# Kernel optimization log

Measured on AMD Instinct MI355X. Metric: run time of the kernel, lower is better.

The kernel has to match this reference:

```python
import jax, jax.numpy as jnp
import numpy as np

KH = KW = 3
STRIDE = 1
PAD = 1
DIL = 1


def _conv2d(x, w, b):
    out = jax.lax.conv_general_dilated(
        x, w, (STRIDE, STRIDE), [(PAD, PAD), (PAD, PAD)],
        rhs_dilation=(DIL, DIL), dimension_numbers=('NCHW', 'OIHW', 'NCHW'))
    return out + b[None, :, None, None]


def _bilinear_sample(x, ys, xs):
    # x: [B,C,H,W]; ys, xs: [B,K,Ho,Wo] float sampling coords (zero padding outside)
    B, C, H, W = x.shape
    y0 = jnp.floor(ys)
    x0 = jnp.floor(xs)
    wy1 = ys - y0
    wx1 = xs - x0
    wy0 = 1.0 - wy1
    wx0 = 1.0 - wx1
    x_flat = x.reshape(B, C, H * W)

    def gather(yc, xc):
        valid = (yc >= 0) & (yc <= H - 1) & (xc >= 0) & (xc <= W - 1)
        yi = jnp.clip(yc, 0, H - 1).astype(jnp.int32)
        xi = jnp.clip(xc, 0, W - 1).astype(jnp.int32)
        idx = yi * W + xi  # [B,K,Ho,Wo]
        g = jax.vmap(lambda xb, ib: xb[:, ib.reshape(-1)])(x_flat, idx)
        g = g.reshape(B, C, *idx.shape[1:])  # [B,C,K,Ho,Wo]
        return g * valid[:, None].astype(x.dtype)

    return (gather(y0, x0) * (wy0 * wx0)[:, None]
            + gather(y0, x0 + 1) * (wy0 * wx1)[:, None]
            + gather(y0 + 1, x0) * (wy1 * wx0)[:, None]
            + gather(y0 + 1, x0 + 1) * (wy1 * wx1)[:, None])


def setup_inputs() -> dict:
    key = jax.random.key(0)
    ks = jax.random.split(key, 6)
    B, C, H, W = 8, 256, 64, 64
    Cout = 256
    K = KH * KW
    x = jax.random.normal(ks[0], (B, C, H, W), jnp.float32)
    # small random offset/mask heads (module inits them to zero; random keeps the
    # irregular-gather path exercised with modest, realistic offsets)
    w_offset = jax.random.normal(ks[1], (2 * K, C, KH, KW), jnp.float32) * 0.01
    b_offset = jax.random.normal(ks[2], (2 * K,), jnp.float32) * 0.1
    w_mask = jax.random.normal(ks[3], (K, C, KH, KW), jnp.float32) * 0.01
    b_mask = jnp.zeros((K,), jnp.float32)
    stdv = 1.0 / np.sqrt(C * KH * KW)
    weight = jax.random.uniform(ks[4], (Cout, C, KH, KW), jnp.float32, -stdv, stdv)
    bias = jnp.zeros((Cout,), jnp.float32)
    return {"x": x, "w_offset": w_offset, "b_offset": b_offset,
            "w_mask": w_mask, "b_mask": b_mask, "weight": weight, "bias": bias}


def reference(x, w_offset, b_offset, w_mask, b_mask, weight, bias):
    B, C, H, W = x.shape
    K = KH * KW
    offset = _conv2d(x, w_offset, b_offset)          # [B, 2K, Ho, Wo]
    mask = jax.nn.sigmoid(_conv2d(x, w_mask, b_mask))  # [B, K, Ho, Wo]
    Ho, Wo = offset.shape[2], offset.shape[3]
    off = offset.reshape(B, K, 2, Ho, Wo)
    dy, dx = off[:, :, 0], off[:, :, 1]              # (dy, dx) pairs per kernel tap
    ky = jnp.arange(KH, dtype=x.dtype) * DIL - PAD
    kx = jnp.arange(KW, dtype=x.dtype) * DIL - PAD
    kyf = jnp.repeat(ky, KW)   # [K]
    kxf = jnp.tile(kx, KH)     # [K]
    ys = jnp.arange(Ho, dtype=x.dtype)[None, None, :, None] * STRIDE + kyf[None, :, None, None] + dy
    xs = jnp.arange(Wo, dtype=x.dtype)[None, None, None, :] * STRIDE + kxf[None, :, None, None] + dx
    sampled = _bilinear_sample(x, ys, xs) * mask[:, None]  # [B,C,K,Ho,Wo]
    out = jnp.einsum('bckhw,ock->bohw', sampled, weight.reshape(weight.shape[0], C, K))
    return out + bias[None, :, None, None]
```

## Files before the change

### kernel.cpp

```cpp
#include <hip/hip_runtime.h>
#include <math.h>


typedef __bf16 bf16x8 __attribute__((ext_vector_type(8)));
typedef float  f32x4  __attribute__((ext_vector_type(4)));
typedef float  f32x2  __attribute__((ext_vector_type(2)));
typedef int    i32x4  __attribute__((ext_vector_type(4)));
typedef unsigned short u16x8 __attribute__((ext_vector_type(8)));
typedef unsigned short u16x4 __attribute__((ext_vector_type(4)));

__device__ __forceinline__ unsigned short f2b(float f) {
  return __builtin_bit_cast(unsigned short, (__bf16)f);
}
__device__ __forceinline__ float blo(unsigned u) {
  return __builtin_bit_cast(float, u << 16);
}
__device__ __forceinline__ float bhi(unsigned u) {
  return __builtin_bit_cast(float, u & 0xffff0000u);
}

__global__ __launch_bounds__(256) void prep(const float* __restrict__ x,
                                            unsigned short* __restrict__ xt,
                                            const float* __restrict__ w,
                                            const float* __restrict__ wo,
                                            const float* __restrict__ wm,
                                            __bf16* __restrict__ wp,
                                            __bf16* __restrict__ womp) {
  __shared__ float tile[64][65];
  const int t = threadIdx.x;
  if (blockIdx.x < 2048) {
    const int bid = blockIdx.x;
    const int b = bid & 7, rem = bid >> 3;
    const int cc = rem & 3, hw0 = (rem >> 2) << 6;
    const int a = t & 63, g = t >> 6;
#pragma unroll
    for (int r = 0; r < 16; ++r) {
      int crow = (r << 2) + g;
      tile[crow][a] = x[(((b << 8) + (cc << 6) + crow) << 12) + hw0 + a];
    }
    __syncthreads();
    const int a0 = (t & 15) << 2, gg = t >> 4;
#pragma unroll
    for (int r = 0; r < 4; ++r) {
      int hwr = (r << 4) + gg;
      u16x4 v;
#pragma unroll
      for (int j = 0; j < 4; ++j) v[j] = f2b(tile[a0 + j][hwr]);
      *(u16x4*)&xt[((b << 12) + hw0 + hwr) * 256 + (cc << 6) + a0] = v;
    }
  } else if (blockIdx.x < 4352) {
    int idx = (blockIdx.x - 2048) * 256 + t;
    int o = idx / 2304, rem = idx - o * 2304;
    int c = rem / 9, k = rem - c * 9;
    wp[(((k << 5) + (c >> 3)) * 256 + o) * 8 + (c & 7)] = (__bf16)w[idx];
  } else {
    int idx = (blockIdx.x - 4352) * 256 + t;
    if (idx >= 32 * 256 * 9) return;
    int r = idx / 2304, rem = idx - r * 2304;
    int c = rem / 9, k = rem - c * 9;
    float v = 0.f;
    if (r < 18) v = wo[((r << 8) + c) * 9 + k];
    else if (r < 27) v = wm[(((r - 18) << 8) + c) * 9 + k];
    womp[(((k << 5) + (c >> 3)) * 32 + r) * 8 + (c & 7)] = (__bf16)v;
  }
}

__global__ __launch_bounds__(512, 2) void deform_fused(
    const unsigned short* __restrict__ xt, const __bf16* __restrict__ wp,
    const __bf16* __restrict__ womp, const float* __restrict__ b_off,
    const float* __restrict__ b_msk, const float* __restrict__ bias,
    float* __restrict__ out) {
  const int bi = blockIdx.x & 7, h = blockIdx.x >> 3;
  const int t = threadIdx.x, lane = t & 63, wv = t >> 6;
  const int l16 = lane & 15, lh = lane >> 4;
  __shared__ __align__(16) unsigned short S[2][64 * 64];
  __shared__ __align__(16) float samp[9][64][8];
  __shared__ __align__(16) float offm[27][64];

  const int sp = t >> 3;
  const int sc0 = (t & 7) << 3;
  const int wofs = (sp << 6) + ((((t & 7) ^ (sp & 7)) & 7) << 3);
  const unsigned short* xtb = xt + ((long)bi << 20);

  {
    f32x4 oacc = {};
    const int mf = wv & 1, nf = wv >> 1;

    auto POLOAD = [&](int it, u16x8* r) {
      const int k = it >> 2, cc = it & 3;
      const int hh = h + k / 3 - 1;
      const int ww = sp + (k % 3) - 1;
      const bool valid = (hh >= 0) & (hh < 64) & (ww >= 0) & (ww < 64);
      if (valid)
        r[0] = *(const u16x8*)(xtb + (((hh << 6) + ww) << 8) + (cc << 6) + sc0);
      else
        r[0] = u16x8{};
    };

    auto POSTEP = [&](int it, const u16x8* r, int buf) {
      *(u16x8*)&S[buf][wofs] = r[0];
      __syncthreads();
      const int k = it >> 2, cc = it & 3;
#pragma unroll
      for (int kk = 0; kk < 2; ++kk) {
        const int prow = (nf << 4) + l16;
        const int gi = (kk << 2) | lh;
        bf16x8 bfrag = *(const bf16x8*)&S[buf][(prow << 6) + (((gi ^ (prow & 7)) & 7) << 3)];
        const __bf16* ap =
            womp + ((((k << 5) + (cc << 3) + (kk << 2) + lh) << 5) + (mf << 4) + l16) * 8;
        bf16x8 af = *(const bf16x8*)ap;
        oacc = __builtin_amdgcn_mfma_f32_16x16x32_bf16(af, bfrag, oacc, 0, 0, 0);
      }
    };

    u16x8 pA[1], pB[1];
    POLOAD(0, pA);
    for (int it = 0; it < 36; it += 2) {
      POLOAD(it + 1, pB);
      POSTEP(it, pA, 0);
      if (it + 2 < 36) POLOAD(it + 2, pA);
      POSTEP(it + 1, pB, 1);
    }

    const int px = (nf << 4) + l16;
#pragma unroll
    for (int r = 0; r < 4; ++r) {
      int row = (mf << 4) + (lh << 2) + r;
      if (row < 18) {
        offm[row][px] = oacc[r] + b_off[row];
      } else if (row < 27) {
        float v = oacc[r] + b_msk[row - 18];
        offm[row][px] = 1.f / (1.f + expf(-v));
      }
    }
    __syncthreads();
  }

  for (int i = t; i < 576; i += 512) {
    int k = i >> 6, p = i & 63;
    float dy = offm[(k << 1)][p], dx = offm[(k << 1) + 1][p], mk = offm[18 + k][p];
    float ys = (float)(h + k / 3 - 1) + dy;
    float xs = (float)(p + k % 3 - 1) + dx;
    float y0f = floorf(ys), x0f = floorf(xs);
    int iy0 = (int)y0f, ix0 = (int)x0f;
    float wy1 = ys - y0f, wx1 = xs - x0f;
    float wy0 = 1.f - wy1, wx0 = 1.f - wx1;
    float w00 = wy0 * wx0 * mk, w01 = wy0 * wx1 * mk;
    float w10 = wy1 * wx0 * mk, w11 = wy1 * wx1 * mk;
    if (iy0 < 0 || iy0 > 63) { w00 = 0.f; w01 = 0.f; }
    if (iy0 < -1 || iy0 > 62) { w10 = 0.f; w11 = 0.f; }
    if (ix0 < 0 || ix0 > 63) { w00 = 0.f; w10 = 0.f; }
    if (ix0 < -1 || ix0 > 62) { w01 = 0.f; w11 = 0.f; }
    const int cy0 = min(max(iy0, 0), 63), cy1 = min(max(iy0 + 1, 0), 63);
    const int cx0 = min(max(ix0, 0), 63), cx1 = min(max(ix0 + 1, 0), 63);
    samp[k][p][0] = w00; samp[k][p][1] = w01;
    samp[k][p][2] = w10; samp[k][p][3] = w11;
    samp[k][p][4] = __builtin_bit_cast(float, (((cy0 << 6) + cx0) << 8));
    samp[k][p][5] = __builtin_bit_cast(float, (((cy0 << 6) + cx1) << 8));
    samp[k][p][6] = __builtin_bit_cast(float, (((cy1 << 6) + cx0) << 8));
    samp[k][p][7] = __builtin_bit_cast(float, (((cy1 << 6) + cx1) << 8));
  }
  __syncthreads();

  f32x4 acc[2][4] = {};

  auto GATHER = [&](int it, u16x8* r, f32x4& w4) {
    const int k = it >> 2, cc = it & 3;
    w4 = *(const f32x4*)&samp[k][sp][0];
    i32x4 o4 = __builtin_bit_cast(i32x4, *(const f32x4*)&samp[k][sp][4]);
    const int c0 = (cc << 6) + sc0;
    r[0] = *(const u16x8*)(xtb + o4.x + c0);
    r[1] = *(const u16x8*)(xtb + o4.y + c0);
    r[2] = *(const u16x8*)(xtb + o4.z + c0);
    r[3] = *(const u16x8*)(xtb + o4.w + c0);
  };

  auto STEP = [&](int it, const u16x8* r, const f32x4& w4, int buf) {
    u16x8 sv;
    const unsigned* u0 = (const unsigned*)&r[0];
    const unsigned* u1 = (const unsigned*)&r[1];
    const unsigned* u2 = (const unsigned*)&r[2];
    const unsigned* u3 = (const unsigned*)&r[3];
#pragma unroll
    for (int j = 0; j < 4; ++j) {
      f32x2 a{blo(u0[j]), bhi(u0[j])};
      f32x2 b{blo(u1[j]), bhi(u1[j])};
      f32x2 c{blo(u2[j]), bhi(u2[j])};
      f32x2 d{blo(u3[j]), bhi(u3[j])};
      f32x2 s = a * w4.x;
      s += b * w4.y;
      s += c * w4.z;
      s += d * w4.w;
      sv[2 * j]     = f2b(s.x);
      sv[2 * j + 1] = f2b(s.y);
    }
    *(u16x8*)&S[buf][wofs] = sv;
    __syncthreads();
    const int k = it >> 2, cc = it & 3;
#pragma unroll
    for (int kk = 0; kk < 2; ++kk) {
      bf16x8 bfr[4];
#pragma unroll
      for (int nf = 0; nf < 4; ++nf) {
        const int prow = (nf << 4) + l16;
        const int gi = (kk << 2) | lh;
        bfr[nf] = *(const bf16x8*)&S[buf][(prow << 6) + (((gi ^ (prow & 7)) & 7) << 3)];
      }
#pragma unroll
      for (int mf = 0; mf < 2; ++mf) {
        const int orow = (wv << 5) + (mf << 4) + l16;
        const __bf16* ap = wp + ((((k << 5) + (cc << 3) + (kk << 2) + lh) << 8) + orow) * 8;
        bf16x8 af = *(const bf16x8*)ap;
#pragma unroll
        for (int nf = 0; nf < 4; ++nf)
          acc[mf][nf] = __builtin_amdgcn_mfma_f32_16x16x32_bf16(af, bfr[nf], acc[mf][nf], 0, 0, 0);
      }
    }
  };

  u16x8 rA[4], rB[4];
  f32x4 wA, wB;
  GATHER(0, rA, wA);
  for (int it = 0; it < 36; it += 2) {
    GATHER(it + 1, rB, wB);
    STEP(it, rA, wA, 0);
    if (it + 2 < 36) GATHER(it + 2, rA, wA);
    STEP(it + 1, rB, wB, 1);
  }

#pragma unroll
  for (int mf = 0; mf < 2; ++mf) {
    const int o = (wv << 5) + (mf << 4) + (lh << 2);
    f32x4 bv = *(const f32x4*)(bias + o);
#pragma unroll
    for (int nf = 0; nf < 4; ++nf) {
      const int p = (nf << 4) + l16;
      const int hw = (h << 6) + p;
#pragma unroll
      for (int r = 0; r < 4; ++r)
        out[(((bi << 8) + o + r) << 12) + hw] = acc[mf][nf][r] + bv[r];
    }
  }
}

extern "C" void kernel_launch(void* const* d_in, const int* in_sizes, int n_in,
                              void* d_out, int out_size, void* d_ws, size_t ws_size,
                              hipStream_t stream) {
  (void)in_sizes; (void)n_in; (void)out_size; (void)ws_size;
  const float* x        = (const float*)d_in[0];
  const float* w_offset = (const float*)d_in[1];
  const float* b_offset = (const float*)d_in[2];
  const float* w_mask   = (const float*)d_in[3];
  const float* b_mask   = (const float*)d_in[4];
  const float* weight   = (const float*)d_in[5];
  const float* bias     = (const float*)d_in[6];
  float* out = (float*)d_out;

  char* ws = (char*)d_ws;
  unsigned short* xt = (unsigned short*)(ws);
  __bf16* Wpack  = (__bf16*)(ws + 16777216);
  __bf16* Womp   = (__bf16*)(ws + 17956864);

  prep<<<4640, 256, 0, stream>>>(x, xt, weight, w_offset, w_mask, Wpack, Womp);
  deform_fused<<<512, 512, 0, stream>>>(xt, Wpack, Womp, b_offset, b_mask, bias, out);
}
```

Measured before the change: 92.00 us.

## Double-buffer offset-conv pipeline in pairs, split MFMA accumulators, halve barriers

Restructures the offset/mask convolution prologue so each step handles two iterations. Two LDS buffer pairs (four buffers) are used, and the next pair's global loads are issued before the current pair's MFMAs. This cuts the barriers from 36 to 18 and stops the LDS store from waiting right before each sync. The two kk MFMAs now write separate accumulators that are summed at the end, which breaks the dependency chain between them. LDS use grows by 16KB per block, which could reduce occupancy under launch_bounds(512,2).

Result: faster. 86.05 us, median of 2 (-6.5%).

```diff
diff --git a/kernel.cpp b/kernel.cpp
--- a/kernel.cpp
+++ b/kernel.cpp
@@ -73,7 +73,7 @@
   const int bi = blockIdx.x & 7, h = blockIdx.x >> 3;
   const int t = threadIdx.x, lane = t & 63, wv = t >> 6;
   const int l16 = lane & 15, lh = lane >> 4;
-  __shared__ __align__(16) unsigned short S[2][64 * 64];
+  __shared__ __align__(16) unsigned short S[4][64 * 64];
   __shared__ __align__(16) float samp[9][64][8];
   __shared__ __align__(16) float offm[27][64];
 
@@ -83,23 +83,18 @@
   const unsigned short* xtb = xt + ((long)bi << 20);
 
   {
-    f32x4 oacc = {};
+    f32x4 oacc0 = {}, oacc1 = {};
     const int mf = wv & 1, nf = wv >> 1;
 
-    auto POLOAD = [&](int it, u16x8* r) {
+    auto PLOAD = [&](int it, u16x8& r) {
       const int k = it >> 2, cc = it & 3;
       const int hh = h + k / 3 - 1;
       const int ww = sp + (k % 3) - 1;
       const bool valid = (hh >= 0) & (hh < 64) & (ww >= 0) & (ww < 64);
-      if (valid)
-        r[0] = *(const u16x8*)(xtb + (((hh << 6) + ww) << 8) + (cc << 6) + sc0);
-      else
-        r[0] = u16x8{};
+      r = valid ? *(const u16x8*)(xtb + (((hh << 6) + ww) << 8) + (cc << 6) + sc0)
+                : u16x8{};
     };
-
-    auto POSTEP = [&](int it, const u16x8* r, int buf) {
-      *(u16x8*)&S[buf][wofs] = r[0];
-      __syncthreads();
+    auto PMFMA = [&](int it, int buf) {
       const int k = it >> 2, cc = it & 3;
 #pragma unroll
       for (int kk = 0; kk < 2; ++kk) {
@@ -109,19 +104,36 @@
         const __bf16* ap =
             womp + ((((k << 5) + (cc << 3) + (kk << 2) + lh) << 5) + (mf << 4) + l16) * 8;
         bf16x8 af = *(const bf16x8*)ap;
-        oacc = __builtin_amdgcn_mfma_f32_16x16x32_bf16(af, bfrag, oacc, 0, 0, 0);
+        if (kk == 0)
+          oacc0 = __builtin_amdgcn_mfma_f32_16x16x32_bf16(af, bfrag, oacc0, 0, 0, 0);
+        else
+          oacc1 = __builtin_amdgcn_mfma_f32_16x16x32_bf16(af, bfrag, oacc1, 0, 0, 0);
       }
     };
 
-    u16x8 pA[1], pB[1];
-    POLOAD(0, pA);
-    for (int it = 0; it < 36; it += 2) {
-      POLOAD(it + 1, pB);
-      POSTEP(it, pA, 0);
-      if (it + 2 < 36) POLOAD(it + 2, pA);
-      POSTEP(it + 1, pB, 1);
-    }
-
+    u16x8 p0, p1;
+    PLOAD(0, p0);
+    PLOAD(1, p1);
+    *(u16x8*)&S[0][wofs] = p0;
+    *(u16x8*)&S[1][wofs] = p1;
+    __syncthreads();
+    for (int p = 0; p < 18; ++p) {
+      const int base = (p & 1) << 1;
+      const int nb = base ^ 2;
+      if (p < 17) {
+        PLOAD((p << 1) + 2, p0);
+        PLOAD((p << 1) + 3, p1);
+      }
+      PMFMA(p << 1, base);
+      PMFMA((p << 1) + 1, base | 1);
+      if (p < 17) {
+        *(u16x8*)&S[nb][wofs] = p0;
+        *(u16x8*)&S[nb | 1][wofs] = p1;
+      }
+      __syncthreads();
+    }
+
+    f32x4 oacc = oacc0 + oacc1;
     const int px = (nf << 4) + l16;
 #pragma unroll
     for (int r = 0; r < 4; ++r) {
```
